# Performance work log

Hardware: AMD Instinct MI355X
Metric: run time of the kernel (lower is better)

The kernel has to match this reference:

```python
import jax, jax.numpy as jnp
import numpy as np

N_NODES = 50000
N_EDGES = 500000
NODE_D = 128
EDGE_D = 128
IN_D = EDGE_D + 2 * NODE_D  # 384


def setup_inputs() -> dict:
    key = jax.random.key(0)
    k1, k2, k3, k4, k5, k6 = jax.random.split(key, 6)
    nodes = jax.random.normal(k1, (N_NODES, NODE_D), dtype=jnp.float32)
    edges = jax.random.normal(k2, (N_EDGES, EDGE_D), dtype=jnp.float32)
    receivers = jax.random.randint(k3, (N_EDGES,), 0, N_NODES, dtype=jnp.int64)
    senders = jax.random.randint(k4, (N_EDGES,), 0, N_NODES, dtype=jnp.int64)
    # Linear(IN_D, EDGE_D): W is [out, in] like torch, b is [out]
    W = jax.random.normal(k5, (EDGE_D, IN_D), dtype=jnp.float32) * (1.0 / np.sqrt(IN_D))
    b = jax.random.normal(k6, (EDGE_D,), dtype=jnp.float32) * 0.01
    return {"nodes": nodes, "edges": edges, "receivers": receivers,
            "senders": senders, "W": W, "b": b}


def reference(nodes, edges, receivers, senders, W, b):
    # gather receiver / sender node features to edges, concat with edge feats
    recv = jnp.take(nodes, receivers, axis=0)   # [E, NODE_D]
    send = jnp.take(nodes, senders, axis=0)     # [E, NODE_D]
    collected = jnp.concatenate([edges, recv, send], axis=-1)  # [E, IN_D]
    updated_edges = collected @ W.T + b          # [E, EDGE_D]
    return updated_edges
```

## Files before the change

kernel.cpp:

```cpp
#include <hip/hip_runtime.h>


#define BM 128
#define NCH 12

typedef __attribute__((ext_vector_type(8))) short bf16x8;
typedef __attribute__((ext_vector_type(4))) float floatx4;
typedef __attribute__((ext_vector_type(4))) unsigned int uint4v;

#define GLOAD_LDS16(g, l) __builtin_amdgcn_global_load_lds(                    \
    (const __attribute__((address_space(1))) unsigned int*)(g),                \
    (__attribute__((address_space(3))) unsigned int*)(l), 16, 0, 0)

static __device__ __forceinline__ unsigned int pack_bf16x2(float lo, float hi) {
    unsigned int a = __builtin_bit_cast(unsigned int, lo);
    unsigned int b = __builtin_bit_cast(unsigned int, hi);
    a += 0x7fffu + ((a >> 16) & 1u);
    b += 0x7fffu + ((b >> 16) & 1u);
    return (a >> 16) | (b & 0xffff0000u);
}

__global__ void cvt_bf16(const float* __restrict__ src, unsigned int* __restrict__ dst, int n4) {
    int i = blockIdx.x * blockDim.x + threadIdx.x;
    if (i < n4) {
        float4 v = ((const float4*)src)[i];
        uint2 p;
        p.x = pack_bf16x2(v.x, v.y);
        p.y = pack_bf16x2(v.z, v.w);
        ((uint2*)dst)[i] = p;
    }
}

__global__ __launch_bounds__(256, 2)
void edge_gemm_v2(const float* __restrict__ edges,
                  const int*   __restrict__ recv,
                  const int*   __restrict__ send,
                  const unsigned short* __restrict__ nodes_bf,
                  const unsigned short* __restrict__ w_bf,
                  const float* __restrict__ bias,
                  float*       __restrict__ out,
                  int E)
{
    __shared__ __align__(16) unsigned short As[2][BM * 32];

    const int tid  = threadIdx.x;
    const int wave = tid >> 6, lane = tid & 63;
    const int quad = lane >> 4, l16 = lane & 15;
    const int wm = (wave >> 1) * 64, wn = (wave & 1) * 64;
    const long e0 = (long)blockIdx.x * BM;

    const int rl   = lane >> 2;
    const int sblk = (lane & 3) ^ ((lane >> 3) & 3);
    long er0 = e0 + wave * 32 + rl;      if (er0 > (long)E - 1) er0 = (long)E - 1;
    long er1 = e0 + wave * 32 + 16 + rl; if (er1 > (long)E - 1) er1 = (long)E - 1;
    const unsigned short* gR0 = nodes_bf + (long)recv[er0] * 128 + sblk * 8;
    const unsigned short* gR1 = nodes_bf + (long)recv[er1] * 128 + sblk * 8;
    const unsigned short* gS0 = nodes_bf + (long)send[er0] * 128 + sblk * 8;
    const unsigned short* gS1 = nodes_bf + (long)send[er1] * 128 + sblk * 8;

    const int erow = tid >> 1;
    long ee = e0 + erow; if (ee > (long)E - 1) ee = (long)E - 1;
    const float* eptr = edges + ee * 128L;
    const int swzE = (erow >> 1) & 3;
    const int b0 = (tid & 1) * 2;
    const int s0 = b0 ^ swzE, s1 = (b0 + 1) ^ swzE;

    floatx4 acc[4][4] = {};
    float4 ev[4];

    auto edge_issue = [&](int c) {
        const float* p = eptr + c * 32;
        ev[0] = *(const float4*)(p + s0 * 8);
        ev[1] = *(const float4*)(p + s0 * 8 + 4);
        ev[2] = *(const float4*)(p + s1 * 8);
        ev[3] = *(const float4*)(p + s1 * 8 + 4);
    };
    auto edge_write = [&](int buf) {
        uint4v w0, w1;
        w0.x = pack_bf16x2(ev[0].x, ev[0].y); w0.y = pack_bf16x2(ev[0].z, ev[0].w);
        w0.z = pack_bf16x2(ev[1].x, ev[1].y); w0.w = pack_bf16x2(ev[1].z, ev[1].w);
        w1.x = pack_bf16x2(ev[2].x, ev[2].y); w1.y = pack_bf16x2(ev[2].z, ev[2].w);
        w1.z = pack_bf16x2(ev[3].x, ev[3].y); w1.w = pack_bf16x2(ev[3].z, ev[3].w);
        *(uint4v*)&As[buf][erow * 32 + b0 * 8]       = w0;
        *(uint4v*)&As[buf][erow * 32 + (b0 + 1) * 8] = w1;
    };
    auto node_issue = [&](int c, int buf) {
        const int off = (c & 3) * 32;
        const unsigned short* g0 = (c < 8) ? gR0 : gS0;
        const unsigned short* g1 = (c < 8) ? gR1 : gS1;
        GLOAD_LDS16(g0 + off, &As[buf][(wave * 2 + 0) * 512]);
        GLOAD_LDS16(g1 + off, &As[buf][(wave * 2 + 1) * 512]);
    };

    bf16x8 bcur[4], bnext[4];
    auto loadB = [&](int c, bf16x8* b) {
        #pragma unroll
        for (int ni = 0; ni < 4; ++ni)
            b[ni] = *(const bf16x8*)(w_bf + (long)(wn + ni * 16 + l16) * 384 + c * 32 + quad * 8);
    };

    edge_issue(0);
    loadB(0, bcur);
    edge_write(0);
    __syncthreads();

    #pragma unroll
    for (int c = 0; c < NCH; ++c) {
        const int buf = c & 1;
        if (c + 1 < NCH) {
            if (c + 1 < 4) edge_issue(c + 1);
            else           node_issue(c + 1, buf ^ 1);
            loadB(c + 1, bnext);
        }
        bf16x8 af[4];
        #pragma unroll
        for (int mi = 0; mi < 4; ++mi)
            af[mi] = *(const bf16x8*)&As[buf][(wm + mi * 16 + l16) * 32 +
                                             ((quad ^ ((l16 >> 1) & 3)) * 8)];
        #pragma unroll
        for (int mi = 0; mi < 4; ++mi)
            #pragma unroll
            for (int ni = 0; ni < 4; ++ni)
                acc[mi][ni] = __builtin_amdgcn_mfma_f32_16x16x32_bf16(
                    af[mi], bcur[ni], acc[mi][ni], 0, 0, 0);
        if (c + 1 < NCH) {
            if (c + 1 < 4) edge_write(buf ^ 1);
            #pragma unroll
            for (int ni = 0; ni < 4; ++ni) bcur[ni] = bnext[ni];
        }
        __syncthreads();
    }

    float bv[4];
    #pragma unroll
    for (int ni = 0; ni < 4; ++ni) bv[ni] = bias[wn + ni * 16 + l16];
    #pragma unroll
    for (int mi = 0; mi < 4; ++mi) {
        #pragma unroll
        for (int r = 0; r < 4; ++r) {
            long row = e0 + wm + mi * 16 + quad * 4 + r;
            if (row < (long)E) {
                float* orow = out + row * 128L + wn + l16;
                #pragma unroll
                for (int ni = 0; ni < 4; ++ni)
                    orow[ni * 16] = acc[mi][ni][r] + bv[ni];
            }
        }
    }
}

#define SA 40
typedef __attribute__((ext_vector_type(8))) short bf16x8f;

__global__ __launch_bounds__(256, 2)
void edgeblock_gemm_fb(const float* __restrict__ nodes,
                       const float* __restrict__ edges,
                       const int*   __restrict__ recv,
                       const int*   __restrict__ send,
                       const float* __restrict__ W,
                       const float* __restrict__ bias,
                       float*       __restrict__ out,
                       int E)
{
    __shared__ __align__(16) unsigned short Asf[2][BM * SA];
    __shared__ __align__(16) unsigned short Bsf[2][BM * SA];
    const int tid = threadIdx.x;
    const int lane8 = tid & 7, h = tid >> 3;
    const int wave = tid >> 6, lane = tid & 63;
    const int quad = lane >> 4, l16 = lane & 15;
    const int wm = (wave >> 1) * 64, wn = (wave & 1) * 64;
    const long e0 = (long)blockIdx.x * BM;
    const float *baseE[4], *baseR[4], *baseS[4];
    #pragma unroll
    for (int i = 0; i < 4; ++i) {
        long e = e0 + h + 32 * i;
        if (e > (long)E - 1) e = (long)E - 1;
        baseE[i] = edges + e * 128L;
        baseR[i] = nodes + (long)recv[e] * 128;
        baseS[i] = nodes + (long)send[e] * 128;
    }
    float4 va[4], vb[4];
    auto loadChunk = [&](int c) {
        const int col = (c & 3) * 32;
        #pragma unroll
        for (int i = 0; i < 4; ++i) {
            const float* src = (c < 4) ? baseE[i] : (c < 8) ? baseR[i] : baseS[i];
            va[i] = *(const float4*)(src + col + lane8 * 4);
            vb[i] = *(const float4*)(W + (long)(h + 32 * i) * 384 + c * 32 + lane8 * 4);
        }
    };
    auto writeChunk = [&](int buf) {
        #pragma unroll
        for (int i = 0; i < 4; ++i) {
            uint2 pa, pb;
            pa.x = pack_bf16x2(va[i].x, va[i].y);
            pa.y = pack_bf16x2(va[i].z, va[i].w);
            pb.x = pack_bf16x2(vb[i].x, vb[i].y);
            pb.y = pack_bf16x2(vb[i].z, vb[i].w);
            *(uint2*)&Asf[buf][(h + 32 * i) * SA + lane8 * 4] = pa;
            *(uint2*)&Bsf[buf][(h + 32 * i) * SA + lane8 * 4] = pb;
        }
    };
    floatx4 acc[4][4] = {};
    loadChunk(0); writeChunk(0); __syncthreads();
    #pragma unroll
    for (int c = 0; c < NCH; ++c) {
        if (c + 1 < NCH) loadChunk(c + 1);
        const int buf = c & 1;
        bf16x8f af[4], bfr[4];
        #pragma unroll
        for (int mi = 0; mi < 4; ++mi)
            af[mi] = *(const bf16x8f*)&Asf[buf][(wm + mi * 16 + l16) * SA + quad * 8];
        #pragma unroll
        for (int ni = 0; ni < 4; ++ni)
            bfr[ni] = *(const bf16x8f*)&Bsf[buf][(wn + ni * 16 + l16) * SA + quad * 8];
        #pragma unroll
        for (int mi = 0; mi < 4; ++mi)
            #pragma unroll
            for (int ni = 0; ni < 4; ++ni)
                acc[mi][ni] = __builtin_amdgcn_mfma_f32_16x16x32_bf16(
                    af[mi], bfr[ni], acc[mi][ni], 0, 0, 0);
        if (c + 1 < NCH) writeChunk((c + 1) & 1);
        __syncthreads();
    }
    float bv[4];
    #pragma unroll
    for (int ni = 0; ni < 4; ++ni) bv[ni] = bias[wn + ni * 16 + l16];
    #pragma unroll
    for (int mi = 0; mi < 4; ++mi)
        #pragma unroll
        for (int r = 0; r < 4; ++r) {
            long row = e0 + wm + mi * 16 + quad * 4 + r;
            if (row < (long)E) {
                float* orow = out + row * 128L + wn + l16;
                #pragma unroll
                for (int ni = 0; ni < 4; ++ni)
                    orow[ni * 16] = acc[mi][ni][r] + bv[ni];
            }
        }
}

extern "C" void kernel_launch(void* const* d_in, const int* in_sizes, int n_in,
                              void* d_out, int out_size, void* d_ws, size_t ws_size,
                              hipStream_t stream) {
    const float* nodes = (const float*)d_in[0];
    const float* edges = (const float*)d_in[1];
    const int*   recv  = (const int*)d_in[2];
    const int*   send  = (const int*)d_in[3];
    const float* W     = (const float*)d_in[4];
    const float* bias  = (const float*)d_in[5];
    float* out = (float*)d_out;

    const int E = in_sizes[2];
    const int grid = (E + BM - 1) / BM;

    const size_t nodes_bytes = (size_t)in_sizes[0] * 2;
    const size_t need = nodes_bytes + (size_t)in_sizes[4] * 2;
    if (ws_size < need) {
        edgeblock_gemm_fb<<<grid, 256, 0, stream>>>(nodes, edges, recv, send, W, bias, out, E);
        return;
    }

    unsigned short* nodes_bf = (unsigned short*)d_ws;
    unsigned short* w_bf     = (unsigned short*)((char*)d_ws + nodes_bytes);

    const int n4n = in_sizes[0] / 4;
    cvt_bf16<<<(n4n + 255) / 256, 256, 0, stream>>>(nodes, (unsigned int*)nodes_bf, n4n);
    const int n4w = in_sizes[4] / 4;
    cvt_bf16<<<(n4w + 255) / 256, 256, 0, stream>>>(W, (unsigned int*)w_bf, n4w);

    edge_gemm_v2<<<grid, 256, 0, stream>>>(edges, recv, send, nodes_bf, w_bf, bias, out, E);
}
```

Before: 528.0 us.

## Shrink edge tile to 32 rows and load all K chunks upfront

Replaces the 128-edge double-buffered K loop with a 32-edge tile. All twelve K chunks (edge features converted to bf16 plus gathered receiver and sender rows) are staged into shared memory at once, followed by a single barrier. Each wave now owns a 32-column slice of the output, and the per-iteration __syncthreads calls are removed. Launch bounds are raised to 6 blocks per CU so more concurrent blocks can hide gather latency. In exchange, each block reloads W from memory four times as often relative to the work it does, and each wave runs fewer MFMAs.

```diff
diff --git a/kernel.cpp b/kernel.cpp
--- a/kernel.cpp
+++ b/kernel.cpp
@@ -1,7 +1,8 @@
 #include <hip/hip_runtime.h>
 
 
-#define BM 128
+#define BM  128
+#define BM3 32
 #define NCH 12
 
 typedef __attribute__((ext_vector_type(8))) short bf16x8;
@@ -31,8 +32,8 @@
     }
 }
 
-__global__ __launch_bounds__(256, 2)
-void edge_gemm_v2(const float* __restrict__ edges,
+__global__ __launch_bounds__(256, 6)
+void edge_gemm_v3(const float* __restrict__ edges,
                   const int*   __restrict__ recv,
                   const int*   __restrict__ send,
                   const unsigned short* __restrict__ nodes_bf,
@@ -41,109 +42,96 @@
                   float*       __restrict__ out,
                   int E)
 {
-    __shared__ __align__(16) unsigned short As[2][BM * 32];
+    __shared__ __align__(16) unsigned short As[NCH][BM3 * 32];
 
     const int tid  = threadIdx.x;
     const int wave = tid >> 6, lane = tid & 63;
     const int quad = lane >> 4, l16 = lane & 15;
-    const int wm = (wave >> 1) * 64, wn = (wave & 1) * 64;
-    const long e0 = (long)blockIdx.x * BM;
+    const int wn = wave * 32;
+    const long e0 = (long)blockIdx.x * BM3;
 
     const int rl   = lane >> 2;
     const int sblk = (lane & 3) ^ ((lane >> 3) & 3);
-    long er0 = e0 + wave * 32 + rl;      if (er0 > (long)E - 1) er0 = (long)E - 1;
-    long er1 = e0 + wave * 32 + 16 + rl; if (er1 > (long)E - 1) er1 = (long)E - 1;
-    const unsigned short* gR0 = nodes_bf + (long)recv[er0] * 128 + sblk * 8;
-    const unsigned short* gR1 = nodes_bf + (long)recv[er1] * 128 + sblk * 8;
-    const unsigned short* gS0 = nodes_bf + (long)send[er0] * 128 + sblk * 8;
-    const unsigned short* gS1 = nodes_bf + (long)send[er1] * 128 + sblk * 8;
-
-    const int erow = tid >> 1;
+    long er = e0 + (wave & 1) * 16 + rl; if (er > (long)E - 1) er = (long)E - 1;
+    const int* idxp = (wave < 2) ? recv : send;
+    const unsigned short* gp = nodes_bf + (long)idxp[er] * 128 + sblk * 8;
+    const int cbase = (wave < 2) ? 4 : 8;
+
+    const int erow = tid >> 3, ep = tid & 7;
     long ee = e0 + erow; if (ee > (long)E - 1) ee = (long)E - 1;
-    const float* eptr = edges + ee * 128L;
-    const int swzE = (erow >> 1) & 3;
-    const int b0 = (tid & 1) * 2;
-    const int s0 = b0 ^ swzE, s1 = (b0 + 1) ^ swzE;
-
-    floatx4 acc[4][4] = {};
+    const float* eptr = edges + ee * 128L + ep * 4;
+    const int ephys = (((ep >> 1) ^ ((erow >> 1) & 3)) * 8) + (ep & 1) * 4;
+
     float4 ev[4];
-
-    auto edge_issue = [&](int c) {
-        const float* p = eptr + c * 32;
-        ev[0] = *(const float4*)(p + s0 * 8);
-        ev[1] = *(const float4*)(p + s0 * 8 + 4);
-        ev[2] = *(const float4*)(p + s1 * 8);
-        ev[3] = *(const float4*)(p + s1 * 8 + 4);
-    };
-    auto edge_write = [&](int buf) {
-        uint4v w0, w1;
-        w0.x = pack_bf16x2(ev[0].x, ev[0].y); w0.y = pack_bf16x2(ev[0].z, ev[0].w);
-        w0.z = pack_bf16x2(ev[1].x, ev[1].y); w0.w = pack_bf16x2(ev[1].z, ev[1].w);
-        w1.x = pack_bf16x2(ev[2].x, ev[2].y); w1.y = pack_bf16x2(ev[2].z, ev[2].w);
-        w1.z = pack_bf16x2(ev[3].x, ev[3].y); w1.w = pack_bf16x2(ev[3].z, ev[3].w);
-        *(uint4v*)&As[buf][erow * 32 + b0 * 8]       = w0;
-        *(uint4v*)&As[buf][erow * 32 + (b0 + 1) * 8] = w1;
-    };
-    auto node_issue = [&](int c, int buf) {
-        const int off = (c & 3) * 32;
-        const unsigned short* g0 = (c < 8) ? gR0 : gS0;
-        const unsigned short* g1 = (c < 8) ? gR1 : gS1;
-        GLOAD_LDS16(g0 + off, &As[buf][(wave * 2 + 0) * 512]);
-        GLOAD_LDS16(g1 + off, &As[buf][(wave * 2 + 1) * 512]);
-    };
-
-    bf16x8 bcur[4], bnext[4];
+    #pragma unroll
+    for (int i = 0; i < 4; ++i) ev[i] = *(const float4*)(eptr + i * 32);
+    #pragma unroll
+    for (int i = 0; i < 4; ++i)
+        GLOAD_LDS16(gp + i * 32, &As[cbase + i][(wave & 1) * 512]);
+
     auto loadB = [&](int c, bf16x8* b) {
         #pragma unroll
-        for (int ni = 0; ni < 4; ++ni)
+        for (int ni = 0; ni < 2; ++ni)
             b[ni] = *(const bf16x8*)(w_bf + (long)(wn + ni * 16 + l16) * 384 + c * 32 + quad * 8);
     };
 
-    edge_issue(0);
+    bf16x8 bcur[2], bnxt[2];
     loadB(0, bcur);
-    edge_write(0);
+    loadB(1, bnxt);
+
+    float bv[2];
+    #pragma unroll
+    for (int ni = 0; ni < 2; ++ni) bv[ni] = bias[wn + ni * 16 + l16];
+
+    #pragma unroll
+    for (int i = 0; i < 4; ++i) {
+        uint2 pw;
+        pw.x = pack_bf16x2(ev[i].x, ev[i].y);
+        pw.y = pack_bf16x2(ev[i].z, ev[i].w);
+        *(uint2*)&As[i][erow * 32 + ephys] = pw;
+    }
+
     __syncthreads();
 
-    #pragma unroll
-    for (int c = 0; c < NCH; ++c) {
-        const int buf = c & 1;
-        if (c + 1 < NCH) {
-            if (c + 1 < 4) edge_issue(c + 1);
-            else           node_issue(c + 1, buf ^ 1);
-            loadB(c + 1, bnext);
-        }
-        bf16x8 af[4];
-        #pragma unroll
-        for (int mi = 0; mi < 4; ++mi)
-            af[mi] = *(const bf16x8*)&As[buf][(wm + mi * 16 + l16) * 32 +
-                                             ((quad ^ ((l16 >> 1) & 3)) * 8)];
-        #pragma unroll
-        for (int mi = 0; mi < 4; ++mi)
+    auto readA = [&](int c, bf16x8* a) {
+        #pragma unroll
+        for (int mi = 0; mi < 2; ++mi)
+            a[mi] = *(const bf16x8*)&As[c][(mi * 16 + l16) * 32 +
+                                           ((quad ^ ((l16 >> 1) & 3)) * 8)];
+    };
+
+    floatx4 acc[2][2] = {};
+    bf16x8 acur[2];
+    readA(0, acur);
+
+    #pragma unroll
+    for (int ks = 0; ks < NCH; ++ks) {
+        bf16x8 an[2], bn[2];
+        if (ks + 2 < NCH) loadB(ks + 2, bn);
+        if (ks + 1 < NCH) readA(ks + 1, an);
+        #pragma unroll
+        for (int mi = 0; mi < 2; ++mi)
             #pragma unroll
-            for (int ni = 0; ni < 4; ++ni)
+            for (int ni = 0; ni < 2; ++ni)
                 acc[mi][ni] = __builtin_amdgcn_mfma_f32_16x16x32_bf16(
-                    af[mi], bcur[ni], acc[mi][ni], 0, 0, 0);
-        if (c + 1 < NCH) {
-            if (c + 1 < 4) edge_write(buf ^ 1);
-            #pragma unroll
-            for (int ni = 0; ni < 4; ++ni) bcur[ni] = bnext[ni];
-        }
-        __syncthreads();
-    }
-
-    float bv[4];
-    #pragma unroll
-    for (int ni = 0; ni < 4; ++ni) bv[ni] = bias[wn + ni * 16 + l16];
-    #pragma unroll
-    for (int mi = 0; mi < 4; ++mi) {
+                    acur[mi], bcur[ni], acc[mi][ni], 0, 0, 0);
+        #pragma unroll
+        for (int i = 0; i < 2; ++i) {
+            if (ks + 1 < NCH) acur[i] = an[i];
+            bcur[i] = bnxt[i];
+            if (ks + 2 < NCH) bnxt[i] = bn[i];
+        }
+    }
+
+    #pragma unroll
+    for (int mi = 0; mi < 2; ++mi) {
         #pragma unroll
         for (int r = 0; r < 4; ++r) {
-            long row = e0 + wm + mi * 16 + quad * 4 + r;
+            long row = e0 + mi * 16 + quad * 4 + r;
             if (row < (long)E) {
                 float* orow = out + row * 128L + wn + l16;
-                #pragma unroll
-                for (int ni = 0; ni < 4; ++ni)
-                    orow[ni * 16] = acc[mi][ni][r] + bv[ni];
+                orow[0]  = acc[mi][0][r] + bv[0];
+                orow[16] = acc[mi][1][r] + bv[1];
             }
         }
     }
@@ -252,12 +240,12 @@
     float* out = (float*)d_out;
 
     const int E = in_sizes[2];
-    const int grid = (E + BM - 1) / BM;
 
     const size_t nodes_bytes = (size_t)in_sizes[0] * 2;
     const size_t need = nodes_bytes + (size_t)in_sizes[4] * 2;
     if (ws_size < need) {
-        edgeblock_gemm_fb<<<grid, 256, 0, stream>>>(nodes, edges, recv, send, W, bias, out, E);
+        const int gridf = (E + BM - 1) / BM;
+        edgeblock_gemm_fb<<<gridf, 256, 0, stream>>>(nodes, edges, recv, send, W, bias, out, E);
         return;
     }
 
@@ -269,5 +257,6 @@
     const int n4w = in_sizes[4] / 4;
     cvt_bf16<<<(n4w + 255) / 256, 256, 0, stream>>>(W, (unsigned int*)w_bf, n4w);
 
-    edge_gemm_v2<<<grid, 256, 0, stream>>>(edges, recv, send, nodes_bf, w_bf, bias, out, E);
-}
+    const int grid = (E + BM3 - 1) / BM3;
+    edge_gemm_v3<<<grid, 256, 0, stream>>>(edges, recv, send, nodes_bf, w_bf, bias, out, E);
+}
```

New measurement: 589.2 us. 11.6% more time.
